# Optimization experiments

Hardware: AMD Instinct MI355X
Metric: run time of the kernel (lower is better)

Reference implementation:

```python
import jax, jax.numpy as jnp
from jax import lax
import numpy as np

NPOINT = 1024   # S: number of sampled centroids
NSAMPLE = 32    # K: neighbors per centroid (unmasked ball query = k-nearest via argsort)


def _gather(p, i):
    # p: [B,N,C], i: [B,...] int -> [B,...,C]
    return jax.vmap(lambda pb, ib: pb[ib])(p, i)


def _fps(xyz, farthest_init, npoint):
    # Iterative farthest point sampling, faithful to the torch loop.
    B, N, _ = xyz.shape
    dist0 = jnp.full((B, N), 1e10, dtype=xyz.dtype)

    def step(carry, _):
        distance, farthest = carry
        centroid = jnp.take_along_axis(xyz, farthest[:, None, None], axis=1)  # [B,1,3]
        d = jnp.sum((xyz - centroid) ** 2, -1)          # [B,N]
        distance = jnp.minimum(distance, d)
        return (distance, jnp.argmax(distance, -1)), farthest

    _, cent = lax.scan(step, (dist0, farthest_init.astype(jnp.int32)), None, length=npoint)
    return cent.T  # [B, npoint]


def _sq_dist(src, dst):
    # src: [B,S,3], dst: [B,N,3] -> [B,S,N]
    return (jnp.sum(src ** 2, -1)[:, :, None]
            + jnp.sum(dst ** 2, -1)[:, None, :]
            - 2.0 * jnp.einsum('bsc,bnc->bsn', src, dst))


def setup_inputs() -> dict:
    key = jax.random.key(0)
    ks = jax.random.split(key, 6)
    B, N, C = 8, 4096, 6
    inp = {
        'xyz': jax.random.normal(ks[0], (B, N, 3), jnp.float32),
        'points': jax.random.normal(ks[1], (B, N, C), jnp.float32),
        'farthest_init': jax.random.randint(ks[2], (B,), 0, N),
    }
    dims = [C + 3, 64, 64, 128]
    for li in range(3):
        inp[f'w{li}'] = jax.random.normal(ks[3 + li], (dims[li + 1], dims[li]), jnp.float32) * 0.1
        inp[f'b{li}'] = jnp.zeros((dims[li + 1],), jnp.float32)
    return inp


def reference(xyz, points, farthest_init, w0, b0, w1, b1, w2, b2):
    fps_idx = _fps(xyz, farthest_init, NPOINT)            # [B,S]
    new_xyz = _gather(xyz, fps_idx)                       # [B,S,3]
    dist = _sq_dist(new_xyz, xyz)                         # [B,S,N]
    _, idx = lax.top_k(-dist, NSAMPLE)                    # k-nearest == argsort[:, :, :K]
    g_xyz = _gather(xyz, idx) - new_xyz[:, :, None, :]    # [B,S,K,3]
    g_pts = _gather(points, idx)                          # [B,S,K,C]
    h = jnp.concatenate([g_xyz, g_pts], axis=-1)          # [B,S,K,C+3]
    for w, b in ((w0, b0), (w1, b1), (w2, b2)):           # 1x1 conv MLP + relu
        h = jax.nn.relu(jnp.einsum('bskc,oc->bsko', h, w) + b)
    new_points = jnp.max(h, axis=2)                       # max-pool over K -> [B,S,128]
    return new_xyz, new_points
```

## Files before the change

### kernel.cpp

```cpp
#include <hip/hip_runtime.h>

#define INF_F 3.402823466e+38f
typedef unsigned long long u64;

__device__ __forceinline__ float f_add(float a, float b){ return __fadd_rn(a,b); }
__device__ __forceinline__ float f_sub(float a, float b){ return __fsub_rn(a,b); }
__device__ __forceinline__ float f_mul(float a, float b){ return __fmul_rn(a,b); }

template<int CTRL>
__device__ __forceinline__ double dpp_d(double x) {
    u64 u = (u64)__double_as_longlong(x);
    int lo = __builtin_amdgcn_update_dpp(0, (int)(unsigned)u,        CTRL, 0xF, 0xF, true);
    int hi = __builtin_amdgcn_update_dpp(0, (int)(unsigned)(u>>32), CTRL, 0xF, 0xF, true);
    return __longlong_as_double((long long)(((u64)(unsigned)hi << 32) | (unsigned)lo));
}

__device__ __forceinline__ double swz16_d(double x) {
    u64 u = (u64)__double_as_longlong(x);
    int lo = __builtin_amdgcn_ds_swizzle((int)(unsigned)u,        0x401F);
    int hi = __builtin_amdgcn_ds_swizzle((int)(unsigned)(u>>32), 0x401F);
    return __longlong_as_double((long long)(((u64)(unsigned)hi << 32) | (unsigned)lo));
}

__global__ __launch_bounds__(256) void fps_kernel(
    const float* __restrict__ xyz, const int* __restrict__ farthest_init,
    float* __restrict__ out_new_xyz)
{
    const int b    = blockIdx.x;
    const int tid  = threadIdx.x;
    const int lane = tid & 63;
    const int wid  = tid >> 6;

    __shared__ float  sx[4096], sy[4096], sz[4096];
    __shared__ int    hist[1024];
    __shared__ double red[2][16];

    const float* xb = xyz + (size_t)b * 4096 * 3;
    for (int n = tid; n < 4096; n += 256) {
        sx[n] = xb[n*3+0]; sy[n] = xb[n*3+1]; sz[n] = xb[n*3+2];
    }
    __syncthreads();

    float px[16], py[16], pz[16], dist[16];
    #pragma unroll
    for (int j = 0; j < 16; ++j) {
        const int n = j * 256 + tid;
        px[j] = sx[n]; py[j] = sy[n]; pz[j] = sz[n];
        dist[j] = 1e10f;
    }
    const unsigned lowbase = 4095u - (unsigned)tid;

    int far = farthest_init[b];
    int p = 0;
    #pragma unroll 1
    for (int it = 0; it < 1024; ++it) {
        if (tid == 0) hist[it] = far;
        const float cx = sx[far], cy = sy[far], cz = sz[far];

        double kk[16];
        #pragma unroll
        for (int j = 0; j < 16; ++j) {
            float dx = f_sub(px[j], cx);
            float dy = f_sub(py[j], cy);
            float dz = f_sub(pz[j], cz);
            float d  = f_add(f_add(f_mul(dx,dx), f_mul(dy,dy)), f_mul(dz,dz));
            float nd = fminf(dist[j], d);
            dist[j] = nd;
            kk[j] = __longlong_as_double((long long)(
                      ((u64)__float_as_uint(nd) << 32) | (u64)(lowbase - 256u*(unsigned)j)));
        }
        #pragma unroll
        for (int st = 8; st; st >>= 1)
            #pragma unroll
            for (int i = 0; i < st; ++i) kk[i] = fmax(kk[i], kk[i+st]);
        double key = kk[0];
        key = fmax(key, dpp_d<0xB1>(key));
        key = fmax(key, dpp_d<0x4E>(key));
        key = fmax(key, dpp_d<0x141>(key));
        key = fmax(key, dpp_d<0x140>(key));
        if ((lane & 15) == 0) red[p][wid*4 + (lane>>4)] = key;
        __syncthreads();
        double r[16];
        #pragma unroll
        for (int i = 0; i < 16; ++i) r[i] = red[p][i];
        #pragma unroll
        for (int st = 8; st; st >>= 1)
            #pragma unroll
            for (int i = 0; i < st; ++i) r[i] = fmax(r[i], r[i+st]);
        far = 4095 - (int)(unsigned)((u64)__double_as_longlong(r[0]) & 0xFFFFFFFFull);
        p ^= 1;
    }
    __syncthreads();
    #pragma unroll
    for (int q = 0; q < 4; ++q) {
        int s  = q * 256 + tid;
        int id = hist[s];
        float* o = out_new_xyz + ((size_t)b * 1024 + s) * 3;
        o[0] = sx[id]; o[1] = sy[id]; o[2] = sz[id];
    }
}

__global__ __launch_bounds__(64) void knn_kernel(
    const float* __restrict__ xyz, const float* __restrict__ new_xyz,
    int* __restrict__ out_idx)
{
    const int blk  = blockIdx.x;
    const int b    = blk >> 10;
    const int lane = threadIdx.x;
    const double DINF = __builtin_huge_val();

    const float* xb = xyz + (size_t)b * 4096 * 3;
    const float* cp = new_xyz + (size_t)blk * 3;
    const float cx = cp[0], cy = cp[1], cz = cp[2];
    const float src2 = f_add(f_add(f_mul(cx,cx), f_mul(cy,cy)), f_mul(cz,cz));

    double key[64];
    #pragma unroll
    for (int j = 0; j < 64; ++j) {
        const int n = j * 64 + lane;
        const float* pt = xb + n * 3;
        float x = pt[0], y = pt[1], z = pt[2];
        float dst2 = f_add(f_add(f_mul(x,x), f_mul(y,y)), f_mul(z,z));
        float dot  = f_add(f_add(f_mul(cx,x), f_mul(cy,y)), f_mul(cz,z));
        float d = f_sub(f_add(src2, dst2), f_mul(2.0f, dot));
        key[j] = __longlong_as_double((long long)(((u64)__float_as_uint(d) << 32) | (u64)(unsigned)n));
    }

    double w = -1.0;
    int myidx = 0;
    #pragma unroll 1
    for (int t = 0; t < 32; ++t) {
        double acc = DINF;
        #pragma unroll
        for (int j = 0; j < 64; ++j) {
            double v = (key[j] > w) ? key[j] : DINF;
            acc = fmin(acc, v);
        }
        acc = fmin(acc, dpp_d<0xB1>(acc));
        acc = fmin(acc, dpp_d<0x4E>(acc));
        acc = fmin(acc, dpp_d<0x141>(acc));
        acc = fmin(acc, dpp_d<0x140>(acc));
        acc = fmin(acc, swz16_d(acc));
        acc = fmin(acc, (double)__shfl_xor(acc, 32));
        if (lane == t) myidx = (int)(unsigned)((u64)__double_as_longlong(acc) & 0xFFFFFFFFull);
        w = acc;
    }
    if (lane < 32) out_idx[(size_t)blk * 32 + lane] = myidx;
}

__global__ __launch_bounds__(256) void mlp_kernel(
    const float* __restrict__ xyz, const float* __restrict__ points,
    const int* __restrict__ knn_idx,
    const float* __restrict__ w0, const float* __restrict__ b0,
    const float* __restrict__ w1, const float* __restrict__ b1,
    const float* __restrict__ w2, const float* __restrict__ b2,
    const float* __restrict__ new_xyz, float* __restrict__ out_np)
{
    const int tid = threadIdx.x;
    const int k   = tid & 31;
    const int gs  = blockIdx.x * 8 + (tid >> 5);
    const int b   = gs >> 10;
    const int n   = knn_idx[(size_t)gs * 32 + k];

    const float cx = new_xyz[gs*3+0], cy = new_xyz[gs*3+1], cz = new_xyz[gs*3+2];
    const float* pxyz = xyz + ((size_t)b * 4096 + n) * 3;
    float h0[9];
    h0[0] = pxyz[0] - cx;
    h0[1] = pxyz[1] - cy;
    h0[2] = pxyz[2] - cz;
    const float* pp = points + ((size_t)b * 4096 + n) * 6;
    #pragma unroll
    for (int c = 0; c < 6; ++c) h0[3 + c] = pp[c];

    float h1[64];
    #pragma unroll
    for (int o = 0; o < 64; ++o) {
        float acc = b0[o];
        #pragma unroll
        for (int c = 0; c < 9; ++c) acc = fmaf(h0[c], w0[o*9+c], acc);
        h1[o] = fmaxf(acc, 0.0f);
    }

    float h2[64];
    #pragma unroll
    for (int o = 0; o < 64; ++o) {
        float acc = b1[o];
        #pragma unroll
        for (int c = 0; c < 64; ++c) acc = fmaf(h1[c], w1[o*64+c], acc);
        h2[o] = fmaxf(acc, 0.0f);
    }

    float* outp = out_np + (size_t)gs * 128;
    for (int og = 0; og < 4; ++og) {
        float keep = 0.0f;
        for (int o2 = 0; o2 < 32; ++o2) {
            const int o = og * 32 + o2;
            float acc = b2[o];
            #pragma unroll
            for (int c = 0; c < 64; ++c) acc = fmaf(h2[c], w2[o*64+c], acc);
            float m = fmaxf(acc, 0.0f);
            #pragma unroll
            for (int mm = 1; mm < 32; mm <<= 1)
                m = fmaxf(m, __shfl_xor(m, mm));
            keep = (k == o2) ? m : keep;
        }
        outp[og * 32 + k] = keep;
    }
}

__global__ __launch_bounds__(256) void knn_mlp_kernel(
    const float* __restrict__ xyz, const float* __restrict__ points,
    const float* __restrict__ w0, const float* __restrict__ b0,
    const float* __restrict__ w1, const float* __restrict__ b1,
    const float* __restrict__ w2, const float* __restrict__ b2,
    const float* __restrict__ new_xyz, float* __restrict__ out_np)
{
    const int blk    = blockIdx.x;
    const int b      = blk >> 7;
    const int s_base = (blk & 127) * 8;
    const int tid    = threadIdx.x;
    const int lane   = tid & 63;
    const int wid    = tid >> 6;

    __shared__ float sx[4096], sy[4096], sz[4096];
    __shared__ float cent[8][3];
    __shared__ int   idxbuf[8][32];

    const float* xb = xyz + (size_t)b * 4096 * 3;
    for (int n = tid; n < 4096; n += 256) {
        sx[n] = xb[n*3+0]; sy[n] = xb[n*3+1]; sz[n] = xb[n*3+2];
    }
    if (tid < 24) ((float*)cent)[tid] = new_xyz[((size_t)b * 1024 + s_base) * 3 + tid];
    __syncthreads();

    for (int si = 0; si < 2; ++si) {
        const int sl = wid * 2 + si;
        const float cx = cent[sl][0], cy = cent[sl][1], cz = cent[sl][2];
        const float src2 = f_add(f_add(f_mul(cx,cx), f_mul(cy,cy)), f_mul(cz,cz));
        float d[64];
        #pragma unroll
        for (int j = 0; j < 64; ++j) {
            int n = j * 64 + lane;
            float x = sx[n], y = sy[n], z = sz[n];
            float dst2 = f_add(f_add(f_mul(x,x), f_mul(y,y)), f_mul(z,z));
            float dot  = f_add(f_add(f_mul(cx,x), f_mul(cy,y)), f_mul(cz,z));
            d[j] = f_sub(f_add(src2, dst2), f_mul(2.0f, dot));
        }
        int myg  = 0;
        int prev = -1;
        for (int t = 0; t < 32; ++t) {
            float bv = INF_F; int bi = 0x7fffffff;
            #pragma unroll
            for (int j = 0; j < 64; ++j) {
                int n = j * 64 + lane;
                if (n == prev) d[j] = INF_F;
                float v = d[j];
                if (v < bv) { bv = v; bi = n; }
            }
            #pragma unroll
            for (int m = 1; m < 64; m <<= 1) {
                float ov = __shfl_xor(bv, m);
                int   oi = __shfl_xor(bi, m);
                if (ov < bv || (ov == bv && oi < bi)) { bv = ov; bi = oi; }
            }
            if (lane == t) myg = bi;
            prev = bi;
        }
        if (lane < 32) idxbuf[sl][lane] = myg;
    }
    __syncthreads();

    const int k   = tid & 31;
    const int sl2 = tid >> 5;
    const int s   = s_base + sl2;
    const int n   = idxbuf[sl2][k];

    const float cx = cent[sl2][0], cy = cent[sl2][1], cz = cent[sl2][2];
    float h0[9];
    h0[0] = sx[n] - cx;
    h0[1] = sy[n] - cy;
    h0[2] = sz[n] - cz;
    const float* pp = points + ((size_t)b * 4096 + n) * 6;
    #pragma unroll
    for (int c = 0; c < 6; ++c) h0[3 + c] = pp[c];

    float h1[64];
    #pragma unroll
    for (int o = 0; o < 64; ++o) {
        float acc = b0[o];
        #pragma unroll
        for (int c = 0; c < 9; ++c) acc = fmaf(h0[c], w0[o*9+c], acc);
        h1[o] = fmaxf(acc, 0.0f);
    }
    float h2[64];
    #pragma unroll
    for (int o = 0; o < 64; ++o) {
        float acc = b1[o];
        #pragma unroll
        for (int c = 0; c < 64; ++c) acc = fmaf(h1[c], w1[o*64+c], acc);
        h2[o] = fmaxf(acc, 0.0f);
    }
    float* outp = out_np + ((size_t)b * 1024 + s) * 128;
    for (int og = 0; og < 4; ++og) {
        float keep = 0.0f;
        for (int o2 = 0; o2 < 32; ++o2) {
            const int o = og * 32 + o2;
            float acc = b2[o];
            #pragma unroll
            for (int c = 0; c < 64; ++c) acc = fmaf(h2[c], w2[o*64+c], acc);
            float m = fmaxf(acc, 0.0f);
            #pragma unroll
            for (int mm = 1; mm < 32; mm <<= 1)
                m = fmaxf(m, __shfl_xor(m, mm));
            keep = (k == o2) ? m : keep;
        }
        outp[og * 32 + k] = keep;
    }
}

extern "C" void kernel_launch(void* const* d_in, const int* in_sizes, int n_in,
                              void* d_out, int out_size, void* d_ws, size_t ws_size,
                              hipStream_t stream) {
    const float* xyz           = (const float*)d_in[0];
    const float* points        = (const float*)d_in[1];
    const int*   farthest_init = (const int*)  d_in[2];
    const float* w0 = (const float*)d_in[3];
    const float* b0 = (const float*)d_in[4];
    const float* w1 = (const float*)d_in[5];
    const float* b1 = (const float*)d_in[6];
    const float* w2 = (const float*)d_in[7];
    const float* b2 = (const float*)d_in[8];

    float* out        = (float*)d_out;
    float* new_xyz    = out;
    float* new_points = out + 8 * 1024 * 3;

    fps_kernel<<<8, 256, 0, stream>>>(xyz, farthest_init, new_xyz);

    if (ws_size >= (size_t)(8192 * 32 * sizeof(int))) {
        int* knn_idx = (int*)d_ws;
        knn_kernel<<<8192, 64, 0, stream>>>(xyz, new_xyz, knn_idx);
        mlp_kernel<<<1024, 256, 0, stream>>>(xyz, points, knn_idx,
                                             w0, b0, w1, b1, w2, b2,
                                             new_xyz, new_points);
    } else {
        knn_mlp_kernel<<<1024, 256, 0, stream>>>(xyz, points, w0, b0, w1, b1, w2, b2,
                                                 new_xyz, new_points);
    }
}
```

Measured before the change: 887.1 us.

## Pack FPS distance math, add group-min kNN selection, use DPP reductions in MLP

FPS now computes two points per packed v_pk_add/v_pk_mul instruction and precomputes the low index bits per slot. The kNN top-32 selection keeps a per-lane minimum for each of eight groups of keys and rescans only the group that held the last winner, instead of all 64 keys every round. kNN also packs four centroids per 256-thread block, and the MLP max-pool over 32 lanes uses DPP and swizzle instead of shfl_xor. The packed math and grouped selection cut VALU work on the FPS and kNN paths, at the cost of inline asm and a switch dispatched through a uniform group id.

```diff
diff --git a/kernel.cpp b/kernel.cpp
--- a/kernel.cpp
+++ b/kernel.cpp
@@ -2,10 +2,14 @@
 
 #define INF_F 3.402823466e+38f
 typedef unsigned long long u64;
+typedef __attribute__((ext_vector_type(2))) float f32x2;
 
 __device__ __forceinline__ float f_add(float a, float b){ return __fadd_rn(a,b); }
 __device__ __forceinline__ float f_sub(float a, float b){ return __fsub_rn(a,b); }
 __device__ __forceinline__ float f_mul(float a, float b){ return __fmul_rn(a,b); }
+
+__device__ __forceinline__ f32x2 pk_add(f32x2 a, f32x2 b){ f32x2 d; asm("v_pk_add_f32 %0, %1, %2" : "=v"(d) : "v"(a), "v"(b)); return d; }
+__device__ __forceinline__ f32x2 pk_mul(f32x2 a, f32x2 b){ f32x2 d; asm("v_pk_mul_f32 %0, %1, %2" : "=v"(d) : "v"(a), "v"(b)); return d; }
 
 template<int CTRL>
 __device__ __forceinline__ double dpp_d(double x) {
@@ -14,11 +18,24 @@
     int hi = __builtin_amdgcn_update_dpp(0, (int)(unsigned)(u>>32), CTRL, 0xF, 0xF, true);
     return __longlong_as_double((long long)(((u64)(unsigned)hi << 32) | (unsigned)lo));
 }
-
+template<int CTRL>
+__device__ __forceinline__ float dpp_f(float x) {
+    int r = __builtin_amdgcn_update_dpp(0, __float_as_int(x), CTRL, 0xF, 0xF, true);
+    return __int_as_float(r);
+}
 __device__ __forceinline__ double swz16_d(double x) {
     u64 u = (u64)__double_as_longlong(x);
     int lo = __builtin_amdgcn_ds_swizzle((int)(unsigned)u,        0x401F);
     int hi = __builtin_amdgcn_ds_swizzle((int)(unsigned)(u>>32), 0x401F);
+    return __longlong_as_double((long long)(((u64)(unsigned)hi << 32) | (unsigned)lo));
+}
+__device__ __forceinline__ float swz16_f(float x) {
+    return __int_as_float(__builtin_amdgcn_ds_swizzle(__float_as_int(x), 0x401F));
+}
+__device__ __forceinline__ double readlane_d(double x, int l) {
+    u64 u = (u64)__double_as_longlong(x);
+    int lo = __builtin_amdgcn_readlane((int)(unsigned)u,        l);
+    int hi = __builtin_amdgcn_readlane((int)(unsigned)(u>>32), l);
     return __longlong_as_double((long long)(((u64)(unsigned)hi << 32) | (unsigned)lo));
 }
 
@@ -41,14 +58,18 @@
     }
     __syncthreads();
 
-    float px[16], py[16], pz[16], dist[16];
-    #pragma unroll
-    for (int j = 0; j < 16; ++j) {
-        const int n = j * 256 + tid;
-        px[j] = sx[n]; py[j] = sy[n]; pz[j] = sz[n];
-        dist[j] = 1e10f;
-    }
-    const unsigned lowbase = 4095u - (unsigned)tid;
+    f32x2 px[8], py[8], pz[8];
+    float dist[16];
+    unsigned lowv[16];
+    #pragma unroll
+    for (int jp = 0; jp < 8; ++jp) {
+        const int n0 = (2*jp) * 256 + tid, n1 = n0 + 256;
+        px[jp] = (f32x2){sx[n0], sx[n1]};
+        py[jp] = (f32x2){sy[n0], sy[n1]};
+        pz[jp] = (f32x2){sz[n0], sz[n1]};
+    }
+    #pragma unroll
+    for (int j = 0; j < 16; ++j) { dist[j] = 1e10f; lowv[j] = 4095u - (unsigned)(j*256 + tid); }
 
     int far = farthest_init[b];
     int p = 0;
@@ -56,18 +77,21 @@
     for (int it = 0; it < 1024; ++it) {
         if (tid == 0) hist[it] = far;
         const float cx = sx[far], cy = sy[far], cz = sz[far];
+        const f32x2 ncx = (f32x2){-cx, -cx};
+        const f32x2 ncy = (f32x2){-cy, -cy};
+        const f32x2 ncz = (f32x2){-cz, -cz};
 
         double kk[16];
         #pragma unroll
-        for (int j = 0; j < 16; ++j) {
-            float dx = f_sub(px[j], cx);
-            float dy = f_sub(py[j], cy);
-            float dz = f_sub(pz[j], cz);
-            float d  = f_add(f_add(f_mul(dx,dx), f_mul(dy,dy)), f_mul(dz,dz));
-            float nd = fminf(dist[j], d);
-            dist[j] = nd;
-            kk[j] = __longlong_as_double((long long)(
-                      ((u64)__float_as_uint(nd) << 32) | (u64)(lowbase - 256u*(unsigned)j)));
+        for (int jp = 0; jp < 8; ++jp) {
+            f32x2 dx = pk_add(px[jp], ncx);
+            f32x2 dy = pk_add(py[jp], ncy);
+            f32x2 dz = pk_add(pz[jp], ncz);
+            f32x2 d2 = pk_add(pk_add(pk_mul(dx,dx), pk_mul(dy,dy)), pk_mul(dz,dz));
+            float nd0 = fminf(dist[2*jp+0], d2.x); dist[2*jp+0] = nd0;
+            float nd1 = fminf(dist[2*jp+1], d2.y); dist[2*jp+1] = nd1;
+            kk[2*jp+0] = __longlong_as_double((long long)(((u64)__float_as_uint(nd0) << 32) | (u64)lowv[2*jp+0]));
+            kk[2*jp+1] = __longlong_as_double((long long)(((u64)__float_as_uint(nd1) << 32) | (u64)lowv[2*jp+1]));
         }
         #pragma unroll
         for (int st = 8; st; st >>= 1)
@@ -100,13 +124,28 @@
     }
 }
 
-__global__ __launch_bounds__(64) void knn_kernel(
+template<int G>
+__device__ __forceinline__ double rebuild8(const double (&key)[64], double w) {
+    const double DINF = __builtin_huge_val();
+    double m = DINF;
+    #pragma unroll
+    for (int e = 0; e < 8; ++e) {
+        double v = key[G*8+e];
+        v = (v > w) ? v : DINF;
+        m = fmin(m, v);
+    }
+    return m;
+}
+
+__global__ __launch_bounds__(256) void knn_kernel(
     const float* __restrict__ xyz, const float* __restrict__ new_xyz,
     int* __restrict__ out_idx)
 {
-    const int blk  = blockIdx.x;
+    const int tid  = threadIdx.x;
+    const int lane = tid & 63;
+    const int wid  = tid >> 6;
+    const int blk  = blockIdx.x * 4 + wid;
     const int b    = blk >> 10;
-    const int lane = threadIdx.x;
     const double DINF = __builtin_huge_val();
 
     const float* xb = xyz + (size_t)b * 4096 * 3;
@@ -126,24 +165,41 @@
         key[j] = __longlong_as_double((long long)(((u64)__float_as_uint(d) << 32) | (u64)(unsigned)n));
     }
 
+    double gm[8];
+    #pragma unroll
+    for (int g = 0; g < 8; ++g) {
+        double m = key[g*8];
+        #pragma unroll
+        for (int e = 1; e < 8; ++e) m = fmin(m, key[g*8+e]);
+        gm[g] = m;
+    }
+
     double w = -1.0;
     int myidx = 0;
     #pragma unroll 1
     for (int t = 0; t < 32; ++t) {
-        double acc = DINF;
-        #pragma unroll
-        for (int j = 0; j < 64; ++j) {
-            double v = (key[j] > w) ? key[j] : DINF;
-            acc = fmin(acc, v);
-        }
-        acc = fmin(acc, dpp_d<0xB1>(acc));
-        acc = fmin(acc, dpp_d<0x4E>(acc));
-        acc = fmin(acc, dpp_d<0x141>(acc));
-        acc = fmin(acc, dpp_d<0x140>(acc));
-        acc = fmin(acc, swz16_d(acc));
-        acc = fmin(acc, (double)__shfl_xor(acc, 32));
-        if (lane == t) myidx = (int)(unsigned)((u64)__double_as_longlong(acc) & 0xFFFFFFFFull);
-        w = acc;
+        double lm = fmin(fmin(fmin(gm[0], gm[1]), fmin(gm[2], gm[3])),
+                         fmin(fmin(gm[4], gm[5]), fmin(gm[6], gm[7])));
+        lm = fmin(lm, dpp_d<0xB1>(lm));
+        lm = fmin(lm, dpp_d<0x4E>(lm));
+        lm = fmin(lm, dpp_d<0x141>(lm));
+        lm = fmin(lm, dpp_d<0x140>(lm));
+        lm = fmin(lm, swz16_d(lm));
+        double gmin = fmin(readlane_d(lm, 0), readlane_d(lm, 32));
+        int n = (int)(unsigned)((u64)__double_as_longlong(gmin) & 0xFFFFFFFFull);
+        if (lane == t) myidx = n;
+        w = gmin;
+        const int gs = __builtin_amdgcn_readfirstlane(n >> 9);
+        switch (gs) {
+            case 0: gm[0] = rebuild8<0>(key, w); break;
+            case 1: gm[1] = rebuild8<1>(key, w); break;
+            case 2: gm[2] = rebuild8<2>(key, w); break;
+            case 3: gm[3] = rebuild8<3>(key, w); break;
+            case 4: gm[4] = rebuild8<4>(key, w); break;
+            case 5: gm[5] = rebuild8<5>(key, w); break;
+            case 6: gm[6] = rebuild8<6>(key, w); break;
+            case 7: gm[7] = rebuild8<7>(key, w); break;
+        }
     }
     if (lane < 32) out_idx[(size_t)blk * 32 + lane] = myidx;
 }
@@ -199,9 +255,11 @@
             #pragma unroll
             for (int c = 0; c < 64; ++c) acc = fmaf(h2[c], w2[o*64+c], acc);
             float m = fmaxf(acc, 0.0f);
-            #pragma unroll
-            for (int mm = 1; mm < 32; mm <<= 1)
-                m = fmaxf(m, __shfl_xor(m, mm));
+            m = fmaxf(m, dpp_f<0xB1>(m));
+            m = fmaxf(m, dpp_f<0x4E>(m));
+            m = fmaxf(m, dpp_f<0x141>(m));
+            m = fmaxf(m, dpp_f<0x140>(m));
+            m = fmaxf(m, swz16_f(m));
             keep = (k == o2) ? m : keep;
         }
         outp[og * 32 + k] = keep;
@@ -339,7 +397,7 @@
 
     if (ws_size >= (size_t)(8192 * 32 * sizeof(int))) {
         int* knn_idx = (int*)d_ws;
-        knn_kernel<<<8192, 64, 0, stream>>>(xyz, new_xyz, knn_idx);
+        knn_kernel<<<2048, 256, 0, stream>>>(xyz, new_xyz, knn_idx);
         mlp_kernel<<<1024, 256, 0, stream>>>(xyz, points, knn_idx,
                                              w0, b0, w1, b1, w2, b2,
                                              new_xyz, new_points);
```

New measurement: 795.6 us. 1.12x faster.
